# Kernel tuning notes

Measured on AMD Instinct MI355X. Metric: run time of the kernel, lower is better.

Reference implementation:

```python
import math
import jax, jax.numpy as jnp
from jax import lax
import numpy as np

B, SEQ, D_MODEL = 8, 1024, 512
R, K, H = 3, 3, 4
DE, DH, DU, DTR, DCONV, DEMB = 64, 64, 32, 4, 3, 10


def setup_inputs() -> dict:
    key = jax.random.key(0)
    ks = iter(jax.random.split(key, 48))
    def nrm(shape, s=0.05):
        return jax.random.normal(next(ks), shape, jnp.float32) * s
    inp = {}
    inp['x'] = jax.random.normal(next(ks), (B, SEQ, D_MODEL), jnp.float32)
    # Mamba params, leading dims (R, 2) = (layer, fwd/bwd direction)
    inp['m_in_w'] = nrm((R, 2, D_MODEL, 2 * DE))
    inp['m_conv_w'] = nrm((R, 2, DE, DCONV), 0.2)
    inp['m_conv_b'] = nrm((R, 2, DE), 0.1)
    inp['m_xproj_w'] = nrm((R, 2, DE, DTR + 2 * DH))
    inp['m_dt_w'] = nrm((R, 2, DTR, DE), 0.2)
    inp['m_dt_b'] = nrm((R, 2, DE), 0.1)
    inp['m_Alog'] = jnp.broadcast_to(jnp.log(jnp.arange(1, DH + 1, dtype=jnp.float32)), (R, 2, DE, DH)) + jnp.zeros((R, 2, DE, DH), jnp.float32)
    inp['m_D'] = jnp.ones((R, 2, DE), jnp.float32)
    inp['m_out_w'] = nrm((R, 2, DE, D_MODEL))
    # LayerNorm / FFN params per layer
    inp['ln1_g'] = jnp.ones((R, D_MODEL), jnp.float32)
    inp['ln1_b'] = jnp.zeros((R, D_MODEL), jnp.float32)
    inp['ffn_w1'] = nrm((R, D_MODEL, DU))
    inp['ffn_b1'] = jnp.zeros((R, DU), jnp.float32)
    inp['ffn_w2'] = nrm((R, DU, D_MODEL))
    inp['ffn_b2'] = jnp.zeros((R, D_MODEL), jnp.float32)
    inp['ln2_g'] = jnp.ones((R, D_MODEL), jnp.float32)
    inp['ln2_b'] = jnp.zeros((R, D_MODEL), jnp.float32)
    # MAGAC params (N = D_MODEL nodes, in_dim = SEQ)
    inp['psi_emb'] = jax.random.normal(next(ks), (D_MODEL, DEMB), jnp.float32)
    inp['psi'] = jnp.array(1.0, jnp.float32)
    inp['W_q'] = jax.random.normal(next(ks), (DEMB, H, DEMB), jnp.float32)
    inp['W_k'] = jax.random.normal(next(ks), (DEMB, H, DEMB), jnp.float32)
    inp['attn_alpha'] = jnp.array(0.5, jnp.float32)
    inp['F_w'] = nrm((H, DEMB, K + 1, SEQ))
    inp['f_b'] = jax.random.normal(next(ks), (H, DEMB), jnp.float32)
    inp['head_mix'] = jnp.ones((H,), jnp.float32)
    inp['head_w'] = nrm((D_MODEL,))
    inp['head_b'] = jnp.zeros((), jnp.float32)
    return inp


def _layernorm(x, g, b, eps=1e-5):
    mu = x.mean(-1, keepdims=True)
    v = ((x - mu) ** 2).mean(-1, keepdims=True)
    return (x - mu) / jnp.sqrt(v + eps) * g + b


def _mamba(x, in_w, conv_w, conv_b, xproj_w, dt_w, dt_b, Alog, Dp, out_w):
    b, l, _ = x.shape
    xr = x @ in_w                              # (b,l,2*DE)
    xp, res = jnp.split(xr, 2, axis=-1)
    # depthwise causal conv (torch pads k-1 both sides then truncates to l == left-pad k-1)
    xc = xp.transpose(0, 2, 1)                 # (b,DE,l)
    xc = lax.conv_general_dilated(xc, conv_w[:, None, :], (1,), [(DCONV - 1, 0)],
                                  feature_group_count=DE,
                                  dimension_numbers=('NCH', 'OIH', 'NCH'))
    xc = xc + conv_b[None, :, None]
    xp = jax.nn.silu(xc.transpose(0, 2, 1))    # (b,l,DE)
    A = -jnp.exp(Alog)                         # (DE,DH)
    x_dbl = xp @ xproj_w                       # (b,l,DTR+2*DH)
    delta = jax.nn.softplus(x_dbl[..., :DTR] @ dt_w + dt_b)   # (b,l,DE)
    Bm = x_dbl[..., DTR:DTR + DH]
    Cm = x_dbl[..., DTR + DH:]
    dA = jnp.exp(delta[..., None] * A)                         # (b,l,DE,DH)
    dBu = delta[..., None] * Bm[:, :, None, :] * xp[..., None] # (b,l,DE,DH)
    def step(s, inp):
        dAt, dBt, ct = inp
        s = dAt * s + dBt
        return s, jnp.einsum('bdn,bn->bd', s, ct)
    s0 = jnp.zeros((b, DE, DH), x.dtype)
    _, ys = lax.scan(step, s0, (dA.transpose(1, 0, 2, 3), dBu.transpose(1, 0, 2, 3), Cm.transpose(1, 0, 2)))
    y = ys.transpose(1, 0, 2) + xp * Dp
    y = y * jax.nn.sigmoid(res)
    return y @ out_w


def _magac(xg, psi_emb, psi, W_q, W_k, attn_alpha, F_w, f_b, head_mix):
    # xg: (B, N, L); eval-mode deterministic path
    diff = psi_emb[:, None, :] - psi_emb[None, :, :]
    A_base = jax.nn.softmax(jnp.exp(-psi * (diff ** 2).sum(-1)), axis=1)   # (N,N)
    Q = jnp.einsum('nd,dhm->nhm', psi_emb, W_q)
    Kq = jnp.einsum('nd,dhm->nhm', psi_emb, W_k)
    attn = jax.nn.softmax(jnp.einsum('nhd,mhd->hnm', Q, Kq) / math.sqrt(DEMB), axis=-1)
    alpha = jax.nn.sigmoid(attn_alpha)
    A_eff = alpha * A_base[None] + (1.0 - alpha) * attn                    # (H,N,N)
    N = psi_emb.shape[0]
    I = jnp.broadcast_to(jnp.eye(N, dtype=xg.dtype), (H, N, N))
    sup = [I, A_eff]
    for _ in range(K - 1):
        sup.append(2.0 * jnp.matmul(A_eff, sup[-1]) - sup[-2])             # Chebyshev
    sup = jnp.stack(sup, axis=1)                                           # (H,K+1,N,N)
    Wf = jnp.einsum('nd,hdkl->hnkl', psi_emb, F_w)                         # (H,N,K+1,L)
    bf = jnp.einsum('nd,hd->hn', psi_emb, f_b)                             # (H,N)
    x_g = jnp.einsum('hknm,bml->bhknl', sup, xg)                           # (B,H,K+1,N,L)
    out_h = jnp.einsum('bhknl,hnkl->bhn', x_g, Wf) + bf[None]
    mix = jax.nn.softmax(head_mix)
    return jnp.einsum('bhn,h->bn', out_h, mix)


def reference(x, m_in_w, m_conv_w, m_conv_b, m_xproj_w, m_dt_w, m_dt_b, m_Alog, m_D, m_out_w,
              ln1_g, ln1_b, ffn_w1, ffn_b1, ffn_w2, ffn_b2, ln2_g, ln2_b,
              psi_emb, psi, W_q, W_k, attn_alpha, F_w, f_b, head_mix, head_w, head_b):
    for i in range(R):
        mf = (m_in_w[i, 0], m_conv_w[i, 0], m_conv_b[i, 0], m_xproj_w[i, 0], m_dt_w[i, 0],
              m_dt_b[i, 0], m_Alog[i, 0], m_D[i, 0], m_out_w[i, 0])
        mb = (m_in_w[i, 1], m_conv_w[i, 1], m_conv_b[i, 1], m_xproj_w[i, 1], m_dt_w[i, 1],
              m_dt_b[i, 1], m_Alog[i, 1], m_D[i, 1], m_out_w[i, 1])
        y_f = _mamba(x, *mf)
        y_b = jnp.flip(_mamba(jnp.flip(x, 1), *mb), 1)
        y = _layernorm(x + y_f + y_b, ln1_g[i], ln1_b[i])
        z = jax.nn.relu(y @ ffn_w1[i] + ffn_b1[i]) @ ffn_w2[i] + ffn_b2[i]
        x = _layernorm(y + z, ln2_g[i], ln2_b[i])
    g = _magac(x.transpose(0, 2, 1), psi_emb, psi, W_q, W_k, attn_alpha, F_w, f_b, head_mix)
    # eval-mode Bayesian MC: all mc_eval samples identical -> mean=g, var=1e-6
    log_var_node = jnp.full_like(g, jnp.log(jnp.asarray(1e-6, g.dtype)))
    mu = g @ head_w + head_b
    var = jnp.exp(log_var_node) @ (head_w ** 2) + 1e-6
    return mu, jnp.log(var)
```

## Files before the change

kernel.cpp:

```cpp
#include <hip/hip_runtime.h>
#include <math.h>

#define SEQL 1024
#define NB 8
#define DMOD 512

__device__ __forceinline__ float blk_sum4(float v, volatile float* sb) {
#pragma unroll
  for (int off = 32; off; off >>= 1) v += __shfl_xor(v, off, 64);
  int lid = threadIdx.x & 63, wid = threadIdx.x >> 6;
  if (lid == 0) sb[wid] = v;
  __syncthreads();
  float t = sb[0] + sb[1] + sb[2] + sb[3];
  __syncthreads();
  return t;
}
__device__ __forceinline__ float blk_max4(float v, volatile float* sb) {
#pragma unroll
  for (int off = 32; off; off >>= 1) v = fmaxf(v, __shfl_xor(v, off, 64));
  int lid = threadIdx.x & 63, wid = threadIdx.x >> 6;
  if (lid == 0) sb[wid] = v;
  __syncthreads();
  float t = fmaxf(fmaxf(sb[0], sb[1]), fmaxf(sb[2], sb[3]));
  __syncthreads();
  return t;
}

__global__ __launch_bounds__(256) void gemm_f32(
    const float* __restrict__ A, long aStr,
    const float* __restrict__ B, long bStr,
    const float* __restrict__ Dm, long dStr,
    float* __restrict__ C, long cStr, long cChunkStr,
    int M, int N, int K, int lda, int ldb, int ldd, int ldc,
    float alpha, float beta, int kchunks) {
  __shared__ float As[2][16][68];
  __shared__ float Bs[2][16][64];
  const int zz = blockIdx.z;
  const int zb = zz / kchunks, kc = zz % kchunks;
  A += (long)zb * aStr + (long)kc * K;
  B += (long)zb * bStr + (long)kc * K * ldb;
  Dm += (long)zb * dStr;
  C += (long)zb * cStr + (long)kc * cChunkStr;
  const int tid = threadIdx.x;
  const int m0 = blockIdx.y * 64, n0 = blockIdx.x * 64;
  const int tx = tid & 15, ty = tid >> 4;
  const int arow = tid >> 2, acol = (tid & 3) << 2;
  const int brow = tid >> 4, bcol = (tid & 15) << 2;
  const bool aOk = (m0 + arow < M);
  const float* Aptr = A + (long)(m0 + arow) * lda + acol;
  const float* Bptr = B + (long)brow * ldb;
  const int bc = n0 + bcol;
  const int kIters = K >> 4;
  float acc[4][4] = {};

  auto loadB = [&](int it) {
    const float* Bk = Bptr + (long)it * 16 * ldb;
    float4 r;
    if (bc + 3 < N) r = *(const float4*)(Bk + bc);
    else {
      r.x = (bc + 0 < N) ? Bk[bc + 0] : 0.f;
      r.y = (bc + 1 < N) ? Bk[bc + 1] : 0.f;
      r.z = (bc + 2 < N) ? Bk[bc + 2] : 0.f;
      r.w = (bc + 3 < N) ? Bk[bc + 3] : 0.f;
    }
    return r;
  };

  float4 av = make_float4(0.f, 0.f, 0.f, 0.f);
  if (aOk) av = *(const float4*)(Aptr);
  float4 bv = loadB(0);
  As[0][acol + 0][arow] = av.x; As[0][acol + 1][arow] = av.y;
  As[0][acol + 2][arow] = av.z; As[0][acol + 3][arow] = av.w;
  *(float4*)&Bs[0][brow][bcol] = bv;

  for (int it = 0; it < kIters; ++it) {
    const int cur = it & 1;
    __syncthreads();
    const bool more = (it + 1 < kIters);
    if (more) {
      if (aOk) av = *(const float4*)(Aptr + (it + 1) * 16);
      bv = loadB(it + 1);
    }
#pragma unroll
    for (int kk = 0; kk < 16; ++kk) {
      float4 aq = *(const float4*)&As[cur][kk][ty << 2];
      float4 bq = *(const float4*)&Bs[cur][kk][tx << 2];
      float aa[4] = {aq.x, aq.y, aq.z, aq.w};
      float bb[4] = {bq.x, bq.y, bq.z, bq.w};
#pragma unroll
      for (int i = 0; i < 4; ++i)
#pragma unroll
        for (int j = 0; j < 4; ++j) acc[i][j] = fmaf(aa[i], bb[j], acc[i][j]);
    }
    if (more) {
      const int nxt = cur ^ 1;
      As[nxt][acol + 0][arow] = av.x; As[nxt][acol + 1][arow] = av.y;
      As[nxt][acol + 2][arow] = av.z; As[nxt][acol + 3][arow] = av.w;
      *(float4*)&Bs[nxt][brow][bcol] = bv;
    }
  }
#pragma unroll
  for (int i = 0; i < 4; ++i) {
    int row = m0 + (ty << 2) + i;
    if (row >= M) continue;
#pragma unroll
    for (int j = 0; j < 4; ++j) {
      int col = n0 + (tx << 2) + j;
      if (col >= N) continue;
      float v = alpha * acc[i][j];
      if (beta != 0.f) v += beta * Dm[(long)row * ldd + col];
      C[(long)row * ldc + col] = v;
    }
  }
}

__global__ __launch_bounds__(256) void convproj(
    const float* __restrict__ xr, const float* __restrict__ cw,
    const float* __restrict__ cb, const float* __restrict__ pw,
    const float* __restrict__ dw, const float* __restrict__ db,
    float* __restrict__ Bm, float* __restrict__ Cm,
    float* __restrict__ xpT, float* __restrict__ dlT, float* __restrict__ sigT) {
  int dir = blockIdx.y;
  int L = blockIdx.x;
  int r = L & 7, q = L >> 3;
  int blk = r * 256 + q;
  int wv = threadIdx.x >> 6, e = threadIdx.x & 63;
  int tok = blk * 4 + wv;
  int b = tok >> 10, t = tok & 1023;
  const float* xrp = xr + (long)dir * 1048576;
  long rb = (long)tok * 128;
  const float* w = cw + dir * 192;
  float w0 = w[e * 3 + 0], w1 = w[e * 3 + 1], w2 = w[e * 3 + 2];
  float acc = cb[dir * 64 + e] + w2 * xrp[rb + e];
  if (dir == 0) {
    if (t >= 1) acc += w1 * xrp[rb - 128 + e];
    if (t >= 2) acc += w0 * xrp[rb - 256 + e];
  } else {
    if (t <= 1022) acc += w1 * xrp[rb + 128 + e];
    if (t <= 1021) acc += w0 * xrp[rb + 256 + e];
  }
  float xpv = acc / (1.f + __expf(-acc));
  float res = xrp[rb + 64 + e];
  float sg = 1.f / (1.f + __expf(-res));
  long tidx = (long)dir * 524288 + (long)b * 65536 + (long)e * 1024 + t;
  xpT[tidx] = xpv;
  sigT[tidx] = sg;
  const float* wp = pw + dir * 8448;
  float aB = 0.f, aC = 0.f, aD = 0.f;
#pragma unroll
  for (int k = 0; k < 64; ++k) {
    float xk = __shfl(xpv, k, 64);
    const float* wr = wp + k * 132;
    aB = fmaf(xk, wr[4 + e], aB);
    aC = fmaf(xk, wr[68 + e], aC);
    aD = fmaf(xk, wr[e & 3], aD);
  }
  long ob = (long)dir * 524288 + (long)tok * 64;
  Bm[ob + e] = aB;
  Cm[ob + e] = aC;
  const float* dwp = dw + dir * 256;
  float dv = db[dir * 64 + e];
#pragma unroll
  for (int rr = 0; rr < 4; ++rr) dv = fmaf(__shfl(aD, rr, 64), dwp[rr * 64 + e], dv);
  dlT[tidx] = fmaxf(dv, 0.f) + log1pf(__expf(-fabsf(dv)));
}

__device__ __forceinline__ void scan_remap(int& d, int& b, int& dir, int& c) {
  int L = blockIdx.x + 64 * (blockIdx.y + 8 * blockIdx.z);
  int r = L & 7, q = L >> 3;
  d = q & 63;
  int T = (q >> 6) * 8 + r;
  b = T >> 5;
  dir = (T >> 4) & 1;
  c = T & 15;
}

__global__ __launch_bounds__(64) void scan_p1(
    const float* __restrict__ dlT, const float* __restrict__ xpT,
    const float* __restrict__ Bm, const float* __restrict__ Alog,
    float* __restrict__ Aprod, float* __restrict__ Send) {
  int d, b, dir, c;
  scan_remap(d, b, dir, c);
  int n = threadIdx.x;
  long tbase = (long)dir * 524288 + (long)b * 65536 + (long)d * 1024;
  int t0 = c * 64;
  float a_dn = -__expf(Alog[dir * 4096 + d * 64 + n]);
  int tg0 = dir ? (1023 - t0) : t0;
  long bstep = dir ? -64 : 64;
  const float* bp = Bm + (long)dir * 524288 + ((long)b * 1024 + tg0) * 64 + n;
  const float* dlrow = dlT + tbase;
  const float* xprow = xpT + tbase;
  float s = 0.f, ap0 = 1.f, ap1 = 1.f;
  for (int sb = 0; sb < 4; ++sb) {
    float sa[16], su[16];
#pragma unroll
    for (int k = 0; k < 16; ++k) {
      int tl = t0 + sb * 16 + k;
      int tg = dir ? 1023 - tl : tl;
      float dv = dlrow[tg];
      sa[k] = dv;
      su[k] = dv * xprow[tg];
    }
#pragma unroll
    for (int k = 0; k < 16; ++k) {
      float bt = bp[(long)k * bstep];
      float a = __expf(sa[k] * a_dn);
      if (k & 1) ap1 *= a; else ap0 *= a;
      s = fmaf(a, s, su[k] * bt);
    }
    bp += 16 * bstep;
  }
  long sidx = ((long)((dir * 8 + b) * 64 + d)) * 1024 + c * 64 + n;
  Aprod[sidx] = ap0 * ap1;
  Send[sidx] = s;
}

__global__ __launch_bounds__(64) void scan_p2(
    const float* __restrict__ Aprod, const float* __restrict__ Send,
    float* __restrict__ Sin) {
  int d = blockIdx.x, b = blockIdx.y, dir = blockIdx.z;
  int n = threadIdx.x;
  long base = ((long)((dir * 8 + b) * 64 + d)) * 1024;
  float apv[16], sev[16];
#pragma unroll
  for (int c = 0; c < 16; ++c) {
    apv[c] = Aprod[base + c * 64 + n];
    sev[c] = Send[base + c * 64 + n];
  }
  float s = 0.f;
#pragma unroll
  for (int c = 0; c < 16; ++c) {
    Sin[base + c * 64 + n] = s;
    s = fmaf(apv[c], s, sev[c]);
  }
}

__global__ __launch_bounds__(64) void scan_p3(
    const float* __restrict__ dlT, const float* __restrict__ xpT,
    const float* __restrict__ sigT, const float* __restrict__ Bm,
    const float* __restrict__ Cm, const float* __restrict__ Alog,
    const float* __restrict__ Dp, const float* __restrict__ Sin,
    float* __restrict__ ycat) {
  __shared__ float sP[16 * 65];
  int d, b, dir, c;
  scan_remap(d, b, dir, c);
  int n = threadIdx.x;
  long tbase = (long)dir * 524288 + (long)b * 65536 + (long)d * 1024;
  int t0 = c * 64;
  int tln = t0 + n;
  int tgn = dir ? 1023 - tln : tln;
  float xp_l = xpT[tbase + tgn];
  float sg_l = sigT[tbase + tgn];
  float a_dn = -__expf(Alog[dir * 4096 + d * 64 + n]);
  float dpd = Dp[dir * 64 + d];
  int tg0 = dir ? (1023 - t0) : t0;
  long bstep = dir ? -64 : 64;
  long boff = (long)dir * 524288 + ((long)b * 1024 + tg0) * 64 + n;
  const float* bp = Bm + boff;
  const float* cp = Cm + boff;
  long sidx = ((long)((dir * 8 + b) * 64 + d)) * 1024 + c * 64 + n;
  float s = Sin[sidx];
  int r4 = n >> 2, q4 = n & 3;
  const float* dlrow = dlT + tbase;
  const float* xprow = xpT + tbase;
  for (int ph = 0; ph < 4; ++ph) {
    float sa[16], su[16];
#pragma unroll
    for (int k = 0; k < 16; ++k) {
      int tl = t0 + ph * 16 + k;
      int tg = dir ? 1023 - tl : tl;
      float dv = dlrow[tg];
      sa[k] = dv;
      su[k] = dv * xprow[tg];
    }
#pragma unroll
    for (int k = 0; k < 16; ++k) {
      float bt = bp[(long)k * bstep];
      float ct = cp[(long)k * bstep];
      float a = __expf(sa[k] * a_dn);
      s = fmaf(a, s, su[k] * bt);
      sP[k * 65 + n] = s * ct;
    }
    bp += 16 * bstep; cp += 16 * bstep;
    __syncthreads();
    float p = 0.f;
#pragma unroll
    for (int k = 0; k < 16; ++k) p += sP[r4 * 65 + q4 * 16 + k];
    p += __shfl_xor(p, 1, 64);
    p += __shfl_xor(p, 2, 64);
    int stl = ph * 16 + r4;
    float xpv_r = __shfl(xp_l, stl, 64);
    float sgv = __shfl(sg_l, stl, 64);
    if (q4 == 0) {
      int tl = t0 + stl;
      int tg = dir ? 1023 - tl : tl;
      ycat[((long)b * 1024 + tg) * 128 + dir * 64 + d] = (p + xpv_r * dpd) * sgv;
    }
    __syncthreads();
  }
}

__global__ __launch_bounds__(256) void ln_ffn_ln(
    float* __restrict__ x, const float* __restrict__ g1, const float* __restrict__ b1v,
    const float* __restrict__ w1, const float* __restrict__ bb1,
    const float* __restrict__ w2, const float* __restrict__ bb2,
    const float* __restrict__ g2, const float* __restrict__ b2v) {
  __shared__ float ybuf[2][512];
  __shared__ float rbuf[2][256];
  __shared__ float zbuf[2][32];
  __shared__ float red4[16];
  int tid = threadIdx.x;
  int lid = tid & 63, wid = tid >> 6;
  float* row0 = x + (long)blockIdx.x * 1024;
  float* row1 = row0 + 512;
  float a0 = row0[tid], b0 = row0[tid + 256];
  float a1 = row1[tid], b1 = row1[tid + 256];
  float s0 = a0 + b0, q0 = a0 * a0 + b0 * b0;
  float s1 = a1 + b1, q1 = a1 * a1 + b1 * b1;
#pragma unroll
  for (int off = 32; off; off >>= 1) {
    s0 += __shfl_xor(s0, off, 64); q0 += __shfl_xor(q0, off, 64);
    s1 += __shfl_xor(s1, off, 64); q1 += __shfl_xor(q1, off, 64);
  }
  if (lid == 0) {
    red4[wid * 4 + 0] = s0; red4[wid * 4 + 1] = q0;
    red4[wid * 4 + 2] = s1; red4[wid * 4 + 3] = q1;
  }
  __syncthreads();
  float S0 = red4[0] + red4[4] + red4[8] + red4[12];
  float Q0 = red4[1] + red4[5] + red4[9] + red4[13];
  float S1 = red4[2] + red4[6] + red4[10] + red4[14];
  float Q1 = red4[3] + red4[7] + red4[11] + red4[15];
  float mu0 = S0 * (1.f / 512.f), mu1 = S1 * (1.f / 512.f);
  float r0 = 1.f / sqrtf(Q0 * (1.f / 512.f) - mu0 * mu0 + 1e-5f);
  float r1 = 1.f / sqrtf(Q1 * (1.f / 512.f) - mu1 * mu1 + 1e-5f);
  float g1a = g1[tid], g1b = g1[tid + 256];
  float b1a = b1v[tid], b1b = b1v[tid + 256];
  float y0a = (a0 - mu0) * r0 * g1a + b1a;
  float y0b = (b0 - mu0) * r0 * g1b + b1b;
  float y1a = (a1 - mu1) * r1 * g1a + b1a;
  float y1b = (b1 - mu1) * r1 * g1b + b1b;
  ybuf[0][tid] = y0a; ybuf[0][tid + 256] = y0b;
  ybuf[1][tid] = y1a; ybuf[1][tid + 256] = y1b;
  __syncthreads();
  int u = tid & 31, seg = tid >> 5;
  int k0 = seg * 64;
  float p0 = 0.f, p1 = 0.f;
#pragma unroll
  for (int k = 0; k < 64; k += 4) {
    float4 ya = *(const float4*)&ybuf[0][k0 + k];
    float4 yb = *(const float4*)&ybuf[1][k0 + k];
    float w1v0 = w1[(k0 + k + 0) * 32 + u];
    float w1v1 = w1[(k0 + k + 1) * 32 + u];
    float w1v2 = w1[(k0 + k + 2) * 32 + u];
    float w1v3 = w1[(k0 + k + 3) * 32 + u];
    p0 = fmaf(ya.w, w1v3, fmaf(ya.z, w1v2, fmaf(ya.y, w1v1, fmaf(ya.x, w1v0, p0))));
    p1 = fmaf(yb.w, w1v3, fmaf(yb.z, w1v2, fmaf(yb.y, w1v1, fmaf(yb.x, w1v0, p1))));
  }
  rbuf[0][seg * 32 + u] = p0;
  rbuf[1][seg * 32 + u] = p1;
  __syncthreads();
  if (tid < 64) {
    int t = tid >> 5, uu = tid & 31;
    float zv = bb1[uu];
#pragma unroll
    for (int sg = 0; sg < 8; ++sg) zv += rbuf[t][sg * 32 + uu];
    zbuf[t][uu] = fmaxf(zv, 0.f);
  }
  __syncthreads();
  float bb2a = bb2[tid], bb2b = bb2[tid + 256];
  float h0a = y0a + bb2a, h0b = y0b + bb2b;
  float h1a = y1a + bb2a, h1b = y1b + bb2b;
#pragma unroll
  for (int uu = 0; uu < 32; ++uu) {
    float wa = w2[uu * 512 + tid], wb = w2[uu * 512 + tid + 256];
    float z0 = zbuf[0][uu], z1 = zbuf[1][uu];
    h0a = fmaf(z0, wa, h0a); h1a = fmaf(z1, wa, h1a);
    h0b = fmaf(z0, wb, h0b); h1b = fmaf(z1, wb, h1b);
  }
  s0 = h0a + h0b; q0 = h0a * h0a + h0b * h0b;
  s1 = h1a + h1b; q1 = h1a * h1a + h1b * h1b;
#pragma unroll
  for (int off = 32; off; off >>= 1) {
    s0 += __shfl_xor(s0, off, 64); q0 += __shfl_xor(q0, off, 64);
    s1 += __shfl_xor(s1, off, 64); q1 += __shfl_xor(q1, off, 64);
  }
  __syncthreads();
  if (lid == 0) {
    red4[wid * 4 + 0] = s0; red4[wid * 4 + 1] = q0;
    red4[wid * 4 + 2] = s1; red4[wid * 4 + 3] = q1;
  }
  __syncthreads();
  S0 = red4[0] + red4[4] + red4[8] + red4[12];
  Q0 = red4[1] + red4[5] + red4[9] + red4[13];
  S1 = red4[2] + red4[6] + red4[10] + red4[14];
  Q1 = red4[3] + red4[7] + red4[11] + red4[15];
  mu0 = S0 * (1.f / 512.f); mu1 = S1 * (1.f / 512.f);
  r0 = 1.f / sqrtf(Q0 * (1.f / 512.f) - mu0 * mu0 + 1e-5f);
  r1 = 1.f / sqrtf(Q1 * (1.f / 512.f) - mu1 * mu1 + 1e-5f);
  float g2a = g2[tid], g2b = g2[tid + 256];
  float b2a = b2v[tid], b2b = b2v[tid + 256];
  row0[tid] = (h0a - mu0) * r0 * g2a + b2a;
  row0[tid + 256] = (h0b - mu0) * r0 * g2b + b2b;
  row1[tid] = (h1a - mu1) * r1 * g2a + b2a;
  row1[tid + 256] = (h1b - mu1) * r1 * g2b + b2b;
}

__global__ __launch_bounds__(64) void qk_kernel(
    const float* __restrict__ e, const float* __restrict__ Wq,
    const float* __restrict__ Wk, float* __restrict__ Qb, float* __restrict__ Kb) {
  int n = blockIdx.x, j = threadIdx.x;
  __shared__ float en[10];
  if (j < 10) en[j] = e[n * 10 + j];
  __syncthreads();
  if (j < 40) {
    float q = 0.f, k = 0.f;
#pragma unroll
    for (int dd = 0; dd < 10; ++dd) {
      q = fmaf(en[dd], Wq[dd * 40 + j], q);
      k = fmaf(en[dd], Wk[dd * 40 + j], k);
    }
    Qb[n * 40 + j] = q;
    Kb[n * 40 + j] = k;
  }
}

__global__ __launch_bounds__(256) void aeff_kernel(
    const float* __restrict__ e, const float* __restrict__ Qb,
    const float* __restrict__ Kb, const float* __restrict__ psi_p,
    const float* __restrict__ alpha_p, float* __restrict__ Aef) {
  int n = blockIdx.x, h = blockIdx.y, tid = threadIdx.x;
  __shared__ float s_at[512];
  __shared__ float s_bs[512];
  __shared__ float qn[10];
  __shared__ float en[10];
  __shared__ float red[4];
  if (tid < 10) { qn[tid] = Qb[n * 40 + h * 10 + tid]; en[tid] = e[n * 10 + tid]; }
  __syncthreads();
  float psi = psi_p[0];
  float alpha = 1.f / (1.f + __expf(-alpha_p[0]));
  const float isq = 0.3162277660168379f;
  for (int m = tid; m < 512; m += 256) {
    float sc = 0.f, d2 = 0.f;
#pragma unroll
    for (int dd = 0; dd < 10; ++dd) {
      sc = fmaf(qn[dd], Kb[m * 40 + h * 10 + dd], sc);
      float df = en[dd] - e[m * 10 + dd];
      d2 = fmaf(df, df, d2);
    }
    s_at[m] = sc * isq;
    s_bs[m] = __expf(-psi * d2);
  }
  __syncthreads();
  float m1 = -1e30f, m2 = -1e30f;
  for (int m = tid; m < 512; m += 256) { m1 = fmaxf(m1, s_at[m]); m2 = fmaxf(m2, s_bs[m]); }
  m1 = blk_max4(m1, red);
  m2 = blk_max4(m2, red);
  float e1 = 0.f, e2 = 0.f;
  for (int m = tid; m < 512; m += 256) {
    float a = __expf(s_at[m] - m1); s_at[m] = a; e1 += a;
    float bq = __expf(s_bs[m] - m2); s_bs[m] = bq; e2 += bq;
  }
  e1 = blk_sum4(e1, red);
  e2 = blk_sum4(e2, red);
  float r1 = (1.f - alpha) / e1, r2 = alpha / e2;
  float* outp = Aef + (long)h * 262144 + (long)n * 512;
  for (int m = tid; m < 512; m += 256) outp[m] = r2 * s_bs[m] + r1 * s_at[m];
}

__global__ void xpose_kernel(const float* __restrict__ DbufP,
                             float* __restrict__ X3, float* __restrict__ X2s,
                             float* __restrict__ X13, float* __restrict__ X02) {
  int idx = blockIdx.x * 256 + threadIdx.x;
  if (idx >= 163840) return;
  int c = idx % 80;
  int m = (idx / 80) % 512;
  int h = idx / 40960;
  int d = c >> 3, b = c & 7;
  long base = (long)(b * 160 + h * 40 + d * 4) * 512 + m;
  float k0 = 0.f, k1 = 0.f, k2 = 0.f, k3 = 0.f;
#pragma unroll
  for (int p = 0; p < 4; ++p) {
    const float* Dp_ = DbufP + (long)p * 655360;
    k0 += Dp_[base];
    k1 += Dp_[base + 512];
    k2 += Dp_[base + 1024];
    k3 += Dp_[base + 1536];
  }
  X3[idx] = k3;
  X2s[idx] = k2;
  X13[idx] = k1 - 3.f * k3;
  X02[idx] = k0 - k2;
}

__global__ void outh_kernel(const float* __restrict__ e, const float* __restrict__ fb,
                            const float* __restrict__ Zt, const float* __restrict__ hm,
                            float* __restrict__ g) {
  int idx = blockIdx.x * 256 + threadIdx.x;
  if (idx >= 4096) return;
  int n = idx & 511, b = idx >> 9;
  float h0 = hm[0], h1 = hm[1], h2 = hm[2], h3 = hm[3];
  float mx = fmaxf(fmaxf(h0, h1), fmaxf(h2, h3));
  float x0 = __expf(h0 - mx), x1 = __expf(h1 - mx), x2 = __expf(h2 - mx), x3 = __expf(h3 - mx);
  float es = x0 + x1 + x2 + x3;
  float mixv[4] = {x0 / es, x1 / es, x2 / es, x3 / es};
  float acc = 0.f;
  for (int h = 0; h < 4; ++h) {
    float oh = 0.f;
#pragma unroll
    for (int dd = 0; dd < 10; ++dd) {
      float ev = e[n * 10 + dd];
      float v = Zt[((long)h * 512 + n) * 80 + dd * 8 + b] + fb[h * 10 + dd];
      oh = fmaf(ev, v, oh);
    }
    acc = fmaf(mixv[h], oh, acc);
  }
  g[b * 512 + n] = acc;
}

__global__ __launch_bounds__(256) void head_kernel(
    const float* __restrict__ g, const float* __restrict__ hw,
    const float* __restrict__ hb, float* __restrict__ out) {
  __shared__ float red[4];
  int b = blockIdx.x, tid = threadIdx.x;
  float w0 = hw[tid], w1 = hw[tid + 256];
  float v = g[b * 512 + tid] * w0 + g[b * 512 + tid + 256] * w1;
  float q = w0 * w0 + w1 * w1;
  float mu = blk_sum4(v, red);
  float s2 = blk_sum4(q, red);
  if (tid == 0) {
    out[b] = mu + hb[0];
    out[8 + b] = logf(1e-6f * s2 + 1e-6f);
  }
}

extern "C" void kernel_launch(void* const* d_in, const int* in_sizes, int n_in,
                              void* d_out, int out_size, void* d_ws, size_t ws_size,
                              hipStream_t stream) {
  (void)in_sizes; (void)n_in; (void)out_size; (void)ws_size;
  const float* x0    = (const float*)d_in[0];
  const float* in_w  = (const float*)d_in[1];
  const float* cw    = (const float*)d_in[2];
  const float* cb    = (const float*)d_in[3];
  const float* pw    = (const float*)d_in[4];
  const float* dtw   = (const float*)d_in[5];
  const float* dtb   = (const float*)d_in[6];
  const float* Alog  = (const float*)d_in[7];
  const float* Dpar  = (const float*)d_in[8];
  const float* ow    = (const float*)d_in[9];
  const float* l1g   = (const float*)d_in[10];
  const float* l1b   = (const float*)d_in[11];
  const float* fw1   = (const float*)d_in[12];
  const float* fb1   = (const float*)d_in[13];
  const float* fw2   = (const float*)d_in[14];
  const float* fb2   = (const float*)d_in[15];
  const float* l2g   = (const float*)d_in[16];
  const float* l2b   = (const float*)d_in[17];
  const float* emb   = (const float*)d_in[18];
  const float* psi   = (const float*)d_in[19];
  const float* Wq    = (const float*)d_in[20];
  const float* Wk    = (const float*)d_in[21];
  const float* aal   = (const float*)d_in[22];
  const float* Fw    = (const float*)d_in[23];
  const float* fbv   = (const float*)d_in[24];
  const float* hmix  = (const float*)d_in[25];
  const float* hw    = (const float*)d_in[26];
  const float* hb    = (const float*)d_in[27];
  float* out = (float*)d_out;

  float* ws = (float*)d_ws;
  float* xA   = ws;
  float* xB   = xA + 4194304;
  float* scr  = xB + 4194304;
  float* xr   = scr;
  float* Bm   = xr + 2097152;
  float* Cm   = Bm + 1048576;
  float* xpT  = Cm + 1048576;
  float* dlT  = xpT + 1048576;
  float* sigT = dlT + 1048576;
  float* ycat = sigT + 1048576;
  float* Sin  = ycat + 1048576;
  float* Aprod = xr;
  float* Send  = xr + 1048576;
  float* Qb    = scr;
  float* Kb    = Qb + 20480;
  float* Aef   = Kb + 20480;
  float* DbufP = Aef + 1048576;
  float* X3    = DbufP + 2621440;
  float* X2s   = X3 + 163840;
  float* X13   = X2s + 163840;
  float* X02   = X13 + 163840;
  float* Z2    = X02 + 163840;
  float* Z1    = Z2 + 163840;
  float* Zt    = Z1 + 163840;
  float* gb    = Zt + 163840;

  const float* xin = x0;
  float* bufs[3] = {xA, xB, xA};
  for (int i = 0; i < 3; ++i) {
    float* xout = bufs[i];
    gemm_f32<<<dim3(2, 128, 2), 256, 0, stream>>>(
        xin, 0, in_w + (long)i * 131072, 65536, xin, 0, xr, 1048576, 0,
        8192, 128, 512, 512, 128, 0, 128, 1.f, 0.f, 1);
    convproj<<<dim3(2048, 2), 256, 0, stream>>>(
        xr, cw + i * 384, cb + i * 128, pw + i * 16896, dtw + i * 512,
        dtb + i * 128, Bm, Cm, xpT, dlT, sigT);
    scan_p1<<<dim3(64, 8, 32), 64, 0, stream>>>(
        dlT, xpT, Bm, Alog + i * 8192, Aprod, Send);
    scan_p2<<<dim3(64, 8, 2), 64, 0, stream>>>(Aprod, Send, Sin);
    scan_p3<<<dim3(64, 8, 32), 64, 0, stream>>>(
        dlT, xpT, sigT, Bm, Cm, Alog + i * 8192, Dpar + i * 128, Sin, ycat);
    gemm_f32<<<dim3(8, 128, 1), 256, 0, stream>>>(
        ycat, 0, ow + (long)i * 65536, 0, xin, 0, xout, 0, 0,
        8192, 512, 128, 128, 512, 512, 512, 1.f, 1.f, 1);
    ln_ffn_ln<<<4096, 256, 0, stream>>>(
        xout, l1g + i * 512, l1b + i * 512, fw1 + i * 16384, fb1 + i * 32,
        fw2 + i * 16384, fb2 + i * 512, l2g + i * 512, l2b + i * 512);
    xin = xout;
  }
  qk_kernel<<<512, 64, 0, stream>>>(emb, Wq, Wk, Qb, Kb);
  aeff_kernel<<<dim3(512, 4), 256, 0, stream>>>(emb, Qb, Kb, psi, aal, Aef);
  gemm_f32<<<dim3(8, 3, 32), 256, 0, stream>>>(
      Fw, 0, xA, 524288, Fw, 0, DbufP, 81920, 655360,
      160, 512, 256, 1024, 512, 0, 512, 1.f, 0.f, 4);
  xpose_kernel<<<640, 256, 0, stream>>>(DbufP, X3, X2s, X13, X02);
  gemm_f32<<<dim3(2, 8, 4), 256, 0, stream>>>(
      Aef, 262144, X3, 40960, X2s, 40960, Z2, 40960, 0,
      512, 80, 512, 512, 80, 80, 80, 4.f, 2.f, 1);
  gemm_f32<<<dim3(2, 8, 4), 256, 0, stream>>>(
      Aef, 262144, Z2, 40960, X13, 40960, Z1, 40960, 0,
      512, 80, 512, 512, 80, 80, 80, 1.f, 1.f, 1);
  gemm_f32<<<dim3(2, 8, 4), 256, 0, stream>>>(
      Aef, 262144, Z1, 40960, X02, 40960, Zt, 40960, 0,
      512, 80, 512, 512, 80, 80, 80, 1.f, 1.f, 1);
  outh_kernel<<<16, 256, 0, stream>>>(emb, fbv, Zt, hmix, gb);
  head_kernel<<<8, 256, 0, stream>>>(gb, hw, hb, out);
}
```

Before: 772.0 us.

## Split-K in-projection, batch 4 tokens per convproj wave, pack scan blocks

The in-projection GEMM is split along K into two halves, written to xr and the xout buffer, and convproj sums the partials on load. convproj now processes four consecutive tokens per wave. This reuses the loaded weights and the conv window across tokens and writes xpT/dlT/sigT as float4 instead of scalar strided stores. The scan kernels pack four independent 64-thread scans into one 256-thread block with per-wave shared buffers, replacing __syncthreads with LDS waitcnt. The costs are extra partial-sum reads, higher register pressure, and reliance on wave-level LDS ordering.

```diff
diff --git a/kernel.cpp b/kernel.cpp
--- a/kernel.cpp
+++ b/kernel.cpp
@@ -115,73 +115,98 @@
 }
 
 __global__ __launch_bounds__(256) void convproj(
-    const float* __restrict__ xr, const float* __restrict__ cw,
-    const float* __restrict__ cb, const float* __restrict__ pw,
-    const float* __restrict__ dw, const float* __restrict__ db,
+    const float* __restrict__ xr0, const float* __restrict__ xr1,
+    const float* __restrict__ cw, const float* __restrict__ cb,
+    const float* __restrict__ pw, const float* __restrict__ dw,
+    const float* __restrict__ db,
     float* __restrict__ Bm, float* __restrict__ Cm,
     float* __restrict__ xpT, float* __restrict__ dlT, float* __restrict__ sigT) {
   int dir = blockIdx.y;
   int L = blockIdx.x;
   int r = L & 7, q = L >> 3;
-  int blk = r * 256 + q;
   int wv = threadIdx.x >> 6, e = threadIdx.x & 63;
-  int tok = blk * 4 + wv;
-  int b = tok >> 10, t = tok & 1023;
-  const float* xrp = xr + (long)dir * 1048576;
-  long rb = (long)tok * 128;
+  int b = r;
+  int t0 = q * 16 + wv * 4;
+  long tokbase = (long)b * 1024;
+  const float* x0p = xr0 + (long)dir * 1048576;
+  const float* x1p = xr1 + (long)dir * 1048576;
+  int base = dir ? t0 : t0 - 2;
+  float X[6];
+#pragma unroll
+  for (int j = 0; j < 6; ++j) {
+    int tt = base + j;
+    if (tt >= 0 && tt <= 1023) {
+      long a = (tokbase + tt) * 128 + e;
+      X[j] = x0p[a] + x1p[a];
+    } else X[j] = 0.f;
+  }
   const float* w = cw + dir * 192;
   float w0 = w[e * 3 + 0], w1 = w[e * 3 + 1], w2 = w[e * 3 + 2];
-  float acc = cb[dir * 64 + e] + w2 * xrp[rb + e];
-  if (dir == 0) {
-    if (t >= 1) acc += w1 * xrp[rb - 128 + e];
-    if (t >= 2) acc += w0 * xrp[rb - 256 + e];
-  } else {
-    if (t <= 1022) acc += w1 * xrp[rb + 128 + e];
-    if (t <= 1021) acc += w0 * xrp[rb + 256 + e];
-  }
-  float xpv = acc / (1.f + __expf(-acc));
-  float res = xrp[rb + 64 + e];
-  float sg = 1.f / (1.f + __expf(-res));
-  long tidx = (long)dir * 524288 + (long)b * 65536 + (long)e * 1024 + t;
-  xpT[tidx] = xpv;
-  sigT[tidx] = sg;
+  float wLo = dir ? w2 : w0;
+  float wHi = dir ? w0 : w2;
+  float cbv = cb[dir * 64 + e];
+  float xpv[4], sg[4];
+#pragma unroll
+  for (int i = 0; i < 4; ++i) {
+    float acc = cbv + wLo * X[i] + w1 * X[i + 1] + wHi * X[i + 2];
+    xpv[i] = acc / (1.f + __expf(-acc));
+    long a = (tokbase + t0 + i) * 128 + 64 + e;
+    float res = x0p[a] + x1p[a];
+    sg[i] = 1.f / (1.f + __expf(-res));
+  }
   const float* wp = pw + dir * 8448;
-  float aB = 0.f, aC = 0.f, aD = 0.f;
-#pragma unroll
+  float aB[4] = {}, aC[4] = {}, aD[4] = {};
   for (int k = 0; k < 64; ++k) {
-    float xk = __shfl(xpv, k, 64);
     const float* wr = wp + k * 132;
-    aB = fmaf(xk, wr[4 + e], aB);
-    aC = fmaf(xk, wr[68 + e], aC);
-    aD = fmaf(xk, wr[e & 3], aD);
-  }
-  long ob = (long)dir * 524288 + (long)tok * 64;
-  Bm[ob + e] = aB;
-  Cm[ob + e] = aC;
+    float wB = wr[4 + e], wC = wr[68 + e], wD = wr[e & 3];
+#pragma unroll
+    for (int i = 0; i < 4; ++i) {
+      float xk = __shfl(xpv[i], k, 64);
+      aB[i] = fmaf(xk, wB, aB[i]);
+      aC[i] = fmaf(xk, wC, aC[i]);
+      aD[i] = fmaf(xk, wD, aD[i]);
+    }
+  }
+  long ob = (long)dir * 524288 + (tokbase + t0) * 64 + e;
+#pragma unroll
+  for (int i = 0; i < 4; ++i) {
+    Bm[ob + (long)i * 64] = aB[i];
+    Cm[ob + (long)i * 64] = aC[i];
+  }
   const float* dwp = dw + dir * 256;
-  float dv = db[dir * 64 + e];
-#pragma unroll
-  for (int rr = 0; rr < 4; ++rr) dv = fmaf(__shfl(aD, rr, 64), dwp[rr * 64 + e], dv);
-  dlT[tidx] = fmaxf(dv, 0.f) + log1pf(__expf(-fabsf(dv)));
-}
-
-__device__ __forceinline__ void scan_remap(int& d, int& b, int& dir, int& c) {
+  float dbv = db[dir * 64 + e];
+  float dl[4];
+#pragma unroll
+  for (int i = 0; i < 4; ++i) {
+    float dv = dbv;
+#pragma unroll
+    for (int rr = 0; rr < 4; ++rr) dv = fmaf(__shfl(aD[i], rr, 64), dwp[rr * 64 + e], dv);
+    dl[i] = fmaxf(dv, 0.f) + log1pf(__expf(-fabsf(dv)));
+  }
+  long tb2 = (long)dir * 524288 + (long)b * 65536 + (long)e * 1024 + t0;
+  *(float4*)&xpT[tb2] = make_float4(xpv[0], xpv[1], xpv[2], xpv[3]);
+  *(float4*)&dlT[tb2] = make_float4(dl[0], dl[1], dl[2], dl[3]);
+  *(float4*)&sigT[tb2] = make_float4(sg[0], sg[1], sg[2], sg[3]);
+}
+
+__device__ __forceinline__ void remap4w(int wv, int& d, int& b, int& dir, int& c) {
   int L = blockIdx.x + 64 * (blockIdx.y + 8 * blockIdx.z);
-  int r = L & 7, q = L >> 3;
-  d = q & 63;
-  int T = (q >> 6) * 8 + r;
+  int r = L & 7, s = L >> 3;
+  int u = s * 4 + wv;
+  d = u & 63;
+  int T = (u >> 6) * 8 + r;
   b = T >> 5;
   dir = (T >> 4) & 1;
   c = T & 15;
 }
 
-__global__ __launch_bounds__(64) void scan_p1(
+__global__ __launch_bounds__(256) void scan_p1(
     const float* __restrict__ dlT, const float* __restrict__ xpT,
     const float* __restrict__ Bm, const float* __restrict__ Alog,
     float* __restrict__ Aprod, float* __restrict__ Send) {
+  int wv = threadIdx.x >> 6, n = threadIdx.x & 63;
   int d, b, dir, c;
-  scan_remap(d, b, dir, c);
-  int n = threadIdx.x;
+  remap4w(wv, d, b, dir, c);
   long tbase = (long)dir * 524288 + (long)b * 65536 + (long)d * 1024;
   int t0 = c * 64;
   float a_dn = -__expf(Alog[dir * 4096 + d * 64 + n]);
@@ -235,16 +260,17 @@
   }
 }
 
-__global__ __launch_bounds__(64) void scan_p3(
+__global__ __launch_bounds__(256) void scan_p3(
     const float* __restrict__ dlT, const float* __restrict__ xpT,
     const float* __restrict__ sigT, const float* __restrict__ Bm,
     const float* __restrict__ Cm, const float* __restrict__ Alog,
     const float* __restrict__ Dp, const float* __restrict__ Sin,
     float* __restrict__ ycat) {
-  __shared__ float sP[16 * 65];
+  __shared__ float sP[4][16 * 65];
+  int wv = threadIdx.x >> 6, n = threadIdx.x & 63;
   int d, b, dir, c;
-  scan_remap(d, b, dir, c);
-  int n = threadIdx.x;
+  remap4w(wv, d, b, dir, c);
+  float* sPw = sP[wv];
   long tbase = (long)dir * 524288 + (long)b * 65536 + (long)d * 1024;
   int t0 = c * 64;
   int tln = t0 + n;
@@ -279,13 +305,13 @@
       float ct = cp[(long)k * bstep];
       float a = __expf(sa[k] * a_dn);
       s = fmaf(a, s, su[k] * bt);
-      sP[k * 65 + n] = s * ct;
+      sPw[k * 65 + n] = s * ct;
     }
     bp += 16 * bstep; cp += 16 * bstep;
-    __syncthreads();
+    asm volatile("s_waitcnt lgkmcnt(0)" ::: "memory");
     float p = 0.f;
 #pragma unroll
-    for (int k = 0; k < 16; ++k) p += sP[r4 * 65 + q4 * 16 + k];
+    for (int k = 0; k < 16; ++k) p += sPw[r4 * 65 + q4 * 16 + k];
     p += __shfl_xor(p, 1, 64);
     p += __shfl_xor(p, 2, 64);
     int stl = ph * 16 + r4;
@@ -296,7 +322,7 @@
       int tg = dir ? 1023 - tl : tl;
       ycat[((long)b * 1024 + tg) * 128 + dir * 64 + d] = (p + xpv_r * dpd) * sgv;
     }
-    __syncthreads();
+    asm volatile("s_waitcnt lgkmcnt(0)" ::: "memory");
   }
 }
 
@@ -599,16 +625,17 @@
   float* bufs[3] = {xA, xB, xA};
   for (int i = 0; i < 3; ++i) {
     float* xout = bufs[i];
-    gemm_f32<<<dim3(2, 128, 2), 256, 0, stream>>>(
-        xin, 0, in_w + (long)i * 131072, 65536, xin, 0, xr, 1048576, 0,
-        8192, 128, 512, 512, 128, 0, 128, 1.f, 0.f, 1);
-    convproj<<<dim3(2048, 2), 256, 0, stream>>>(
-        xr, cw + i * 384, cb + i * 128, pw + i * 16896, dtw + i * 512,
+    gemm_f32<<<dim3(2, 128, 4), 256, 0, stream>>>(
+        xin, 0, in_w + (long)i * 131072, 65536, xin, 0, xr, 1048576,
+        (long)(xout - xr),
+        8192, 128, 256, 512, 128, 0, 128, 1.f, 0.f, 2);
+    convproj<<<dim3(512, 2), 256, 0, stream>>>(
+        xr, xout, cw + i * 384, cb + i * 128, pw + i * 16896, dtw + i * 512,
         dtb + i * 128, Bm, Cm, xpT, dlT, sigT);
-    scan_p1<<<dim3(64, 8, 32), 64, 0, stream>>>(
+    scan_p1<<<dim3(64, 8, 8), 256, 0, stream>>>(
         dlT, xpT, Bm, Alog + i * 8192, Aprod, Send);
     scan_p2<<<dim3(64, 8, 2), 64, 0, stream>>>(Aprod, Send, Sin);
-    scan_p3<<<dim3(64, 8, 32), 64, 0, stream>>>(
+    scan_p3<<<dim3(64, 8, 8), 256, 0, stream>>>(
         dlT, xpT, sigT, Bm, Cm, Alog + i * 8192, Dpar + i * 128, Sin, ycat);
     gemm_f32<<<dim3(8, 128, 1), 256, 0, stream>>>(
         ycat, 0, ow + (long)i * 65536, 0, xin, 0, xout, 0, 0,
```

New measurement: 857.6 us. 1.11x slower.
